# Optimization experiments

Hardware: AMD Instinct MI355X
Metric: run time of the kernel (lower is better)

## Reference

```python
import jax, jax.numpy as jnp
import numpy as np

N_HEADS = 16


def setup_inputs() -> dict:
    key = jax.random.key(0)
    ks = jax.random.split(key, 11)
    B, S, D = 4, 2048, 1024
    scale = 1.0 / np.sqrt(D)
    inp = {
        "xq": jax.random.normal(ks[0], (B, S, D), jnp.float32),
        "xk": jax.random.normal(ks[1], (B, S, D), jnp.float32),
        "xv": jax.random.normal(ks[2], (B, S, D), jnp.float32),
        "wq": jax.random.normal(ks[3], (D, D), jnp.float32) * scale,
        "bq": jnp.zeros((D,), jnp.float32),
        "wk": jax.random.normal(ks[4], (D, D), jnp.float32) * scale,
        "bk": jnp.zeros((D,), jnp.float32),
        "wv": jax.random.normal(ks[5], (D, D), jnp.float32) * scale,
        "bv": jnp.zeros((D,), jnp.float32),
        "wo": jax.random.normal(ks[6], (D, D), jnp.float32) * scale,
        "bo": jnp.zeros((D,), jnp.float32),
    }
    return inp


def reference(xq, xk, xv, wq, bq, wk, bk, wv, bv, wo, bo):
    B, S, D = xq.shape
    H = N_HEADS
    dh = D // H

    def split_heads(x):
        # (B, S, D) -> (B, H, S, dh)
        return x.reshape(B, S, H, dh).transpose(0, 2, 1, 3)

    q = split_heads(xq @ wq + bq)
    k = split_heads(xk @ wk + bk)
    v = split_heads(xv @ wv + bv)

    # FFT-based autocorrelation along the sequence axis (axis=2)
    q_fft = jnp.fft.rfft(q, axis=2)
    k_fft = jnp.fft.rfft(k, axis=2)
    autocorr = jnp.fft.irfft(q_fft * jnp.conj(k_fft), n=S, axis=2)  # (B,H,S,dh)
    scaled = autocorr / jnp.sqrt(jnp.float32(dh))

    # top-k delay selection over mean correlation across channel dim
    k_top = max(S // 5, 1)
    mean_corr = scaled.mean(axis=-1)  # (B,H,S)
    top_values, top_indices = jax.lax.top_k(mean_corr, k_top)  # (B,H,K)

    # gather values at top delays: (B,H,K,dh)
    v_sel = jnp.take_along_axis(v, top_indices[..., None], axis=2)
    weights = jax.nn.softmax(top_values, axis=-1)  # (B,H,K)
    attended = jnp.einsum('bhk,bhkd->bhd', weights, v_sel)  # (B,H,dh)

    # broadcast across seq, merge heads, output projection
    out = jnp.broadcast_to(attended[:, :, None, :], (B, H, S, dh))
    out = out.transpose(0, 2, 1, 3).reshape(B, S, D)
    return out @ wo + bo
```

## Files before the change

### kernel.cpp

```cpp
#include <hip/hip_runtime.h>
#include <math.h>

#define SB 4
#define SS 2048
#define SD 1024
#define SH 16
#define KTOP 409
#define KSL 8
#define KPS 52

typedef float f32x4  __attribute__((ext_vector_type(4)));
typedef short bf16x8 __attribute__((ext_vector_type(8)));
typedef short s16x4  __attribute__((ext_vector_type(4)));

__device__ __forceinline__ short f2bf(float x) {
  unsigned u = __float_as_uint(x);
  u += 0x7fff + ((u >> 16) & 1);
  return (short)(u >> 16);
}
__device__ __forceinline__ float bf2f(short s) {
  return __uint_as_float(((unsigned)(unsigned short)s) << 16);
}

__device__ __forceinline__ void gld16(const void* g, void* l) {
  __builtin_amdgcn_global_load_lds(
      (const __attribute__((address_space(1))) void*)g,
      (__attribute__((address_space(3))) void*)l, 16, 0, 0);
}

#define XS(i) ((i) ^ ((((i) >> 4) ^ ((i) >> 8)) & 15))

template<int SIGN>
__device__ __forceinline__ void fft2048_lds(float2* z, const float2* tw, int tid) {
#pragma unroll
  for (int l = 0; l < 4; ++l) {
    int bf = tid + l * 256;
    int i0 = XS(2 * bf), i1 = XS(2 * bf + 1);
    float2 a = z[i0], b = z[i1];
    z[i0] = make_float2(a.x + b.x, a.y + b.y);
    z[i1] = make_float2(a.x - b.x, a.y - b.y);
  }
  __syncthreads();
#pragma unroll
  for (int lq = 1; lq <= 9; lq += 2) {
    const int q = 1 << lq;
#pragma unroll
    for (int l = 0; l < 2; ++l) {
      int bf = tid + l * 256;
      int p = bf & (q - 1);
      int base = ((bf >> lq) << (lq + 2)) + p;
      int e1 = p << (9 - lq);
      int e2 = e1 << 1;
      int e3 = e1 * 3;
      float2 w1 = tw[XS(e1)];
      float2 w2 = tw[XS(e2)];
      float s3 = 1.f; int e3w = e3;
      if (e3 >= 1024) { e3w = e3 - 1024; s3 = -1.f; }
      float2 w3 = tw[XS(e3w)]; w3.x *= s3; w3.y *= s3;
      float2 t0 = z[XS(base)];
      float2 vb = z[XS(base + 2 * q)];
      float2 vc = z[XS(base + q)];
      float2 vd = z[XS(base + 3 * q)];
      float w1i = SIGN * w1.y, w2i = SIGN * w2.y, w3i = SIGN * w3.y;
      float2 t1 = make_float2(vb.x * w1.x - vb.y * w1i, vb.x * w1i + vb.y * w1.x);
      float2 t2 = make_float2(vc.x * w2.x - vc.y * w2i, vc.x * w2i + vc.y * w2.x);
      float2 t3 = make_float2(vd.x * w3.x - vd.y * w3i, vd.x * w3i + vd.y * w3.x);
      float2 s02 = make_float2(t0.x + t2.x, t0.y + t2.y);
      float2 d02 = make_float2(t0.x - t2.x, t0.y - t2.y);
      float2 s13 = make_float2(t1.x + t3.x, t1.y + t3.y);
      float2 d13 = make_float2(t1.x - t3.x, t1.y - t3.y);
      float2 r13 = make_float2(SIGN * d13.y, -SIGN * d13.x);
      z[XS(base)]         = make_float2(s02.x + s13.x, s02.y + s13.y);
      z[XS(base + q)]     = make_float2(d02.x + r13.x, d02.y + r13.y);
      z[XS(base + 2 * q)] = make_float2(s02.x - s13.x, s02.y - s13.y);
      z[XS(base + 3 * q)] = make_float2(d02.x - r13.x, d02.y - r13.y);
    }
    __syncthreads();
  }
}

template<int SIGN>
__device__ __forceinline__ void fft2048x2_lds(
    float2* __restrict__ z0, float2* __restrict__ z1,
    const float2* tw, int tid)
{
#pragma unroll
  for (int l = 0; l < 4; ++l) {
    int bf = tid + l * 256;
    int i0 = XS(2 * bf), i1 = XS(2 * bf + 1);
    float2 a0 = z0[i0], b0 = z0[i1];
    float2 a1 = z1[i0], b1 = z1[i1];
    z0[i0] = make_float2(a0.x + b0.x, a0.y + b0.y);
    z0[i1] = make_float2(a0.x - b0.x, a0.y - b0.y);
    z1[i0] = make_float2(a1.x + b1.x, a1.y + b1.y);
    z1[i1] = make_float2(a1.x - b1.x, a1.y - b1.y);
  }
  __syncthreads();
#pragma unroll
  for (int lq = 1; lq <= 9; lq += 2) {
    const int q = 1 << lq;
#pragma unroll
    for (int l = 0; l < 2; ++l) {
      int bf = tid + l * 256;
      int p = bf & (q - 1);
      int base = ((bf >> lq) << (lq + 2)) + p;
      int e1 = p << (9 - lq);
      int e2 = e1 << 1;
      int e3 = e1 * 3;
      float2 w1 = tw[XS(e1)];
      float2 w2 = tw[XS(e2)];
      float s3 = 1.f; int e3w = e3;
      if (e3 >= 1024) { e3w = e3 - 1024; s3 = -1.f; }
      float2 w3 = tw[XS(e3w)]; w3.x *= s3; w3.y *= s3;
      float w1i = SIGN * w1.y, w2i = SIGN * w2.y, w3i = SIGN * w3.y;
      const int ia = XS(base), ib = XS(base + 2 * q),
                ic = XS(base + q), id = XS(base + 3 * q);
#pragma unroll
      for (int s = 0; s < 2; ++s) {
        float2* z = s ? z1 : z0;
        float2 t0 = z[ia];
        float2 vb = z[ib];
        float2 vc = z[ic];
        float2 vd = z[id];
        float2 t1 = make_float2(vb.x * w1.x - vb.y * w1i, vb.x * w1i + vb.y * w1.x);
        float2 t2 = make_float2(vc.x * w2.x - vc.y * w2i, vc.x * w2i + vc.y * w2.x);
        float2 t3 = make_float2(vd.x * w3.x - vd.y * w3i, vd.x * w3i + vd.y * w3.x);
        float2 s02 = make_float2(t0.x + t2.x, t0.y + t2.y);
        float2 d02 = make_float2(t0.x - t2.x, t0.y - t2.y);
        float2 s13 = make_float2(t1.x + t3.x, t1.y + t3.y);
        float2 d13 = make_float2(t1.x - t3.x, t1.y - t3.y);
        float2 r13 = make_float2(SIGN * d13.y, -SIGN * d13.x);
        z[ia] = make_float2(s02.x + s13.x, s02.y + s13.y);
        z[ic] = make_float2(d02.x + r13.x, d02.y + r13.y);
        z[ib] = make_float2(s02.x - s13.x, s02.y - s13.y);
        z[id] = make_float2(d02.x - r13.x, d02.y - r13.y);
      }
    }
    __syncthreads();
  }
}

__global__ __launch_bounds__(256) void twiddle_k(float2* __restrict__ twtab) {
  int j = blockIdx.x * 256 + threadIdx.x;
  float a = 6.2831853071795864769f * (float)j / 2048.0f;
  twtab[j] = make_float2(cosf(a), -sinf(a));
}

__global__ __launch_bounds__(256) void splitwt_k(
    const float* __restrict__ wq, const float* __restrict__ wk,
    short* __restrict__ wqt, short* __restrict__ wkt)
{
  const float* W = blockIdx.z ? wk : wq;
  short* Wt = blockIdx.z ? wkt : wqt;
  const int n0 = blockIdx.x * 64, k0 = blockIdx.y * 64;
  __shared__ float T[64][65];
  const int tid = threadIdx.x;
#pragma unroll
  for (int l = 0; l < 4; ++l) {
    int idx = tid + l * 256;
    int r = idx >> 4, c4 = (idx & 15) << 2;
    float4 v = *(const float4*)&W[(size_t)(k0 + r) * SD + n0 + c4];
    T[r][c4 + 0] = v.x; T[r][c4 + 1] = v.y; T[r][c4 + 2] = v.z; T[r][c4 + 3] = v.w;
  }
  __syncthreads();
#pragma unroll
  for (int l = 0; l < 4; ++l) {
    int idx = tid + l * 256;
    int nr = idx >> 4, k4 = (idx & 15) << 2;
    s16x4 hi, lo;
#pragma unroll
    for (int j = 0; j < 4; ++j) {
      float x = T[k4 + j][nr];
      short hb = f2bf(x);
      hi[j] = hb; lo[j] = f2bf(x - bf2f(hb));
    }
    int ks = (((k4 >> 3) ^ (nr & 7)) << 3) | (k4 & 7);
    *(s16x4*)&Wt[(size_t)(n0 + nr) * 2048 + k0 + ks] = hi;
    *(s16x4*)&Wt[(size_t)(n0 + nr) * 2048 + 1024 + k0 + ks] = lo;
  }
}

__global__ __launch_bounds__(256) void splitx2_k(
    const float* __restrict__ Xq, const float* __restrict__ Xk,
    short* __restrict__ Xqh, short* __restrict__ Xql,
    short* __restrict__ Xkh, short* __restrict__ Xkl)
{
  const int tid = threadIdx.x;
  const int row = blockIdx.x * 2 + (tid >> 7);
  const int G = tid & 127;
  const float* X = blockIdx.y ? Xk : Xq;
  short* Xh = blockIdx.y ? Xkh : Xqh;
  short* Xl = blockIdx.y ? Xkl : Xql;
  const float* src = X + ((size_t)row << 10) + (G << 3);
  float4 a = *(const float4*)src;
  float4 b = *(const float4*)(src + 4);
  float xs[8] = {a.x, a.y, a.z, a.w, b.x, b.y, b.z, b.w};
  bf16x8 hi, lo;
#pragma unroll
  for (int j = 0; j < 8; ++j) {
    short hb = f2bf(xs[j]);
    hi[j] = hb; lo[j] = f2bf(xs[j] - bf2f(hb));
  }
  int Gd = (G & 0x78) | ((G ^ row) & 7);
  size_t d = ((size_t)row << 10) + (Gd << 3);
  *(bf16x8*)&Xh[d] = hi;
  *(bf16x8*)&Xl[d] = lo;
}

__global__ __launch_bounds__(256) void projm_k(
    const short* __restrict__ Xqh, const short* __restrict__ Xql,
    const short* __restrict__ Wq_, const float* __restrict__ bq_,
    float* __restrict__ Oq_,
    const short* __restrict__ Xkh, const short* __restrict__ Xkl,
    const short* __restrict__ Wk_, const float* __restrict__ bk_,
    float* __restrict__ Ok_, int ldT)
{
  const int total = gridDim.x * gridDim.y * gridDim.z;
  int g = blockIdx.x + gridDim.x * (blockIdx.y + gridDim.y * blockIdx.z);
  int t = ((total & 7) == 0) ? (((g & 7) * (total >> 3)) + (g >> 3)) : g;
  const int nb = t % gridDim.x;
  int tmp = t / gridDim.x;
  const int mb = tmp % gridDim.y;
  const int zb = tmp / gridDim.y;

  const short* Xh; const short* Xl; const short* Wt; const float* bias; float* Out;
  if (zb == 0) { Xh = Xqh; Xl = Xql; Wt = Wq_; bias = bq_; Out = Oq_; }
  else         { Xh = Xkh; Xl = Xkl; Wt = Wk_; bias = bk_; Out = Ok_; }
  const int n0 = nb * 128, m0 = mb * 128;
  __shared__ __align__(16) short Ah[128 * 64];
  __shared__ __align__(16) short Al[128 * 64];
  __shared__ __align__(16) short Bh[128 * 64];
  __shared__ __align__(16) short Bl[128 * 64];
  const int tid = threadIdx.x;
  const int wave = tid >> 6, lane = tid & 63, l15 = lane & 15, kq = lane >> 4;
  const int wr = wave >> 1, wc = wave & 1;
  const int sr = lane >> 3, sc = lane & 7;
  f32x4 acc[4][4];
#pragma unroll
  for (int i = 0; i < 4; ++i)
#pragma unroll
    for (int j = 0; j < 4; ++j)
#pragma unroll
      for (int r = 0; r < 4; ++r) acc[i][j][r] = 0.f;
  float bval[4];
#pragma unroll
  for (int j = 0; j < 4; ++j) bval[j] = bias[n0 + wc * 64 + j * 16 + l15];

  for (int s = 0; s < 16; ++s) {
    __syncthreads();
#pragma unroll
    for (int l = 0; l < 4; ++l) {
      int rr = l * 32 + wave * 8 + sr;
      int lofs = (l * 32 + wave * 8) * 64;
      size_t gA = ((size_t)(m0 + rr) << 10) + (s << 6) + (sc << 3);
      gld16(Xh + gA, Ah + lofs);
      gld16(Xl + gA, Al + lofs);
      size_t gB = ((size_t)(n0 + rr) << 11) + (s << 6) + (sc << 3);
      gld16(Wt + gB, Bh + lofs);
      gld16(Wt + gB + 1024, Bl + lofs);
    }
    __syncthreads();
#pragma unroll
    for (int ks = 0; ks < 2; ++ks) {
      int seg = ks * 4 + kq;
      bf16x8 ah[4], al[4], bh[4], bl[4];
#pragma unroll
      for (int i = 0; i < 4; ++i) {
        int ar = wr * 64 + i * 16 + l15;
        int addr = ar * 64 + ((seg ^ (ar & 7)) << 3);
        ah[i] = *(const bf16x8*)&Ah[addr];
        al[i] = *(const bf16x8*)&Al[addr];
      }
#pragma unroll
      for (int j = 0; j < 4; ++j) {
        int br = wc * 64 + j * 16 + l15;
        int addr = br * 64 + ((seg ^ (br & 7)) << 3);
        bh[j] = *(const bf16x8*)&Bh[addr];
        bl[j] = *(const bf16x8*)&Bl[addr];
      }
#pragma unroll
      for (int i = 0; i < 4; ++i)
#pragma unroll
        for (int j = 0; j < 4; ++j) {
          acc[i][j] = __builtin_amdgcn_mfma_f32_16x16x32_bf16(ah[i], bh[j], acc[i][j], 0, 0, 0);
          acc[i][j] = __builtin_amdgcn_mfma_f32_16x16x32_bf16(al[i], bh[j], acc[i][j], 0, 0, 0);
          acc[i][j] = __builtin_amdgcn_mfma_f32_16x16x32_bf16(ah[i], bl[j], acc[i][j], 0, 0, 0);
        }
    }
  }
#pragma unroll
  for (int i = 0; i < 4; ++i)
#pragma unroll
    for (int j = 0; j < 4; ++j) {
      int n = n0 + wc * 64 + j * 16 + l15;
      int tb = m0 + wr * 64 + i * 16 + kq * 4;
      float4 v = make_float4(acc[i][j][0] + bval[j], acc[i][j][1] + bval[j],
                             acc[i][j][2] + bval[j], acc[i][j][3] + bval[j]);
      *(float4*)&Out[(size_t)n * ldT + tb] = v;
    }
}

__global__ __launch_bounds__(256) void fftcorr_k(
    const float* __restrict__ Qt, const float* __restrict__ Kt,
    float* __restrict__ Pat, float2* __restrict__ Ppart,
    const float2* __restrict__ twtab, int ld)
{
  const int dg = blockIdx.x, h = blockIdx.y, b = blockIdx.z;
  const size_t bofs = (size_t)b * SS;
  __shared__ float2 z0[2048];
  __shared__ float2 z1[2048];
  __shared__ float2 tw[1024];
  const int tid = threadIdx.x;
  for (int j = tid; j < 1024; j += 256) tw[XS(j)] = twtab[j];
  float prr[8], pii[8];
#pragma unroll
  for (int l = 0; l < 8; ++l) { prr[l] = 0.f; pii[l] = 0.f; }

  for (int dd = 0; dd < 4; ++dd) {
    const int n = h * 64 + dg * 8 + dd * 2;
    const float2* q0 = (const float2*)(Qt + (size_t)n * ld + bofs);
    const float2* k0 = (const float2*)(Kt + (size_t)n * ld + bofs);
    const float2* q1 = (const float2*)(Qt + (size_t)(n + 1) * ld + bofs);
    const float2* k1 = (const float2*)(Kt + (size_t)(n + 1) * ld + bofs);
    __syncthreads();
#pragma unroll
    for (int l = 0; l < 4; ++l) {
      int t2 = tid + l * 256;
      int t = 2 * t2;
      int rv = __brev((unsigned)t) >> 21;
      int zia = XS(rv);
      int zib = XS(rv + 1024);
      float2 fq0 = q0[t2], fk0 = k0[t2];
      float2 fq1 = q1[t2], fk1 = k1[t2];
      z0[zia] = make_float2(fq0.x, fk0.x);
      z0[zib] = make_float2(fq0.y, fk0.y);
      z1[zia] = make_float2(fq1.x, fk1.x);
      z1[zib] = make_float2(fq1.y, fk1.y);
    }
    __syncthreads();
    fft2048x2_lds<1>(z0, z1, tw, tid);
#pragma unroll
    for (int l = 0; l < 8; ++l) {
      int f = tid + l * 256;
      int fc = (2048 - f) & 2047;
#pragma unroll
      for (int s = 0; s < 2; ++s) {
        const float2* z = s ? z1 : z0;
        float2 Z = z[XS(f)];
        float2 Zc = z[XS(fc)];
        float Zcr = Zc.x, Zci = -Zc.y;
        float Qr = 0.5f * (Z.x + Zcr), Qi = 0.5f * (Z.y + Zci);
        float Kr = 0.5f * (Z.y - Zci), Ki = -0.5f * (Z.x - Zcr);
        prr[l] += Qr * Kr + Qi * Ki;
        pii[l] += Qi * Kr - Qr * Ki;
      }
    }
  }
  if (Ppart) {
    float2* Pp = Ppart + ((size_t)dg * 64 + (size_t)b * SH + h) * 2048;
#pragma unroll
    for (int l = 0; l < 8; ++l) {
      int f = tid + l * 256;
      Pp[f] = make_float2(prr[l], pii[l]);
    }
  } else {
    float* Pb = Pat;
#pragma unroll
    for (int l = 0; l < 8; ++l) {
      int f = tid + l * 256;
      atomicAdd(&Pb[((size_t)h * SS + f) * 2 + 0], prr[l]);
      atomicAdd(&Pb[((size_t)h * SS + f) * 2 + 1], pii[l]);
    }
  }
}

__global__ __launch_bounds__(256) void ifft_topk_k(
    const float* __restrict__ P, const float2* __restrict__ Ppart, int nparts,
    const float2* __restrict__ twtab,
    int* __restrict__ sidx, float* __restrict__ sw)
{
  const int bh = blockIdx.x;
  __shared__ float2 z[2048];
  __shared__ float2 tw[1024];
  __shared__ unsigned keys[2048];
  __shared__ int el_i[KTOP];
  __shared__ float el_w[KTOP];
  __shared__ int hist[256];
  __shared__ int scan_sh[256];
  __shared__ int wtot[4];
  __shared__ int cnt2, tiecnt, sel_v;
  __shared__ unsigned kmax_sh;
  __shared__ float Zsh;
  const int tid = threadIdx.x;
  const int lane = tid & 63, wv = tid >> 6;
  const float SCL = 1.0f / (2048.0f * 512.0f);

  for (int j = tid; j < 1024; j += 256) tw[XS(j)] = twtab[j];
  if (tid == 0) { cnt2 = 0; tiecnt = 0; kmax_sh = 0u; Zsh = 0.f; }
#pragma unroll
  for (int l = 0; l < 8; ++l) {
    int f = tid + l * 256;
    int rv = __brev((unsigned)f) >> 21;
    float2 acc;
    if (nparts > 0) {
      acc = make_float2(0.f, 0.f);
      for (int g = 0; g < nparts; ++g) {
        float2 v = Ppart[((size_t)g * 64 + bh) * 2048 + f];
        acc.x += v.x; acc.y += v.y;
      }
    } else {
      acc = ((const float2*)P)[(size_t)bh * SS + f];
    }
    z[XS(rv)] = acc;
  }
  __syncthreads();
  fft2048_lds<-1>(z, tw, tid);

  unsigned lm = 0u;
#pragma unroll
  for (int l = 0; l < 8; ++l) {
    int i = tid + l * 256;
    float v = z[XS(i)].x * SCL;
    z[XS(i)].x = v;
    unsigned u = __float_as_uint(v);
    unsigned k = (u & 0x80000000u) ? ~u : (u | 0x80000000u);
    keys[i] = k;
    lm = max(lm, k);
  }
  atomicMax(&kmax_sh, lm);
  __syncthreads();

  unsigned prefix = 0u;
  int remaining = KTOP;
  for (int p = 3; p >= 0; --p) {
    hist[tid] = 0;
    __syncthreads();
    unsigned mask_hi = (p == 3) ? 0u : (0xFFFFFFFFu << ((p + 1) * 8));
#pragma unroll
    for (int l = 0; l < 8; ++l) {
      unsigned k = keys[tid + l * 256];
      if ((k & mask_hi) == prefix) atomicAdd(&hist[(k >> (p * 8)) & 255], 1);
    }
    __syncthreads();
    int v = hist[tid];
#pragma unroll
    for (int off2 = 1; off2 < 64; off2 <<= 1) {
      int t = __shfl_down(v, off2);
      if (lane + off2 < 64) v += t;
    }
    if (lane == 0) wtot[wv] = v;
    __syncthreads();
    for (int w = wv + 1; w < 4; ++w) v += wtot[w];
    scan_sh[tid] = v;
    __syncthreads();
    if (scan_sh[tid] >= remaining && (tid == 255 || scan_sh[tid + 1] < remaining))
      sel_v = tid;
    __syncthreads();
    int vsel = sel_v;
    int above = (vsel == 255) ? 0 : scan_sh[vsel + 1];
    remaining -= above;
    prefix |= ((unsigned)vsel) << (p * 8);
    __syncthreads();
  }
  const unsigned T = prefix;
  unsigned km = kmax_sh;
  float vmax = __uint_as_float((km & 0x80000000u) ? (km ^ 0x80000000u) : ~km);

#pragma unroll
  for (int l = 0; l < 8; ++l) {
    int i = tid + l * 256;
    unsigned k = keys[i];
    if (k > T) {
      int pos = atomicAdd(&cnt2, 1);
      el_i[pos] = i;
      el_w[pos] = expf(z[XS(i)].x - vmax);
    } else if (k == T) {
      atomicAdd(&tiecnt, 1);
    }
  }
  __syncthreads();
  int need = KTOP - cnt2;
  if (tiecnt == need) {
#pragma unroll
    for (int l = 0; l < 8; ++l) {
      int i = tid + l * 256;
      if (keys[i] == T) {
        int pos = atomicAdd(&cnt2, 1);
        el_i[pos] = i;
        el_w[pos] = expf(z[XS(i)].x - vmax);
      }
    }
  } else if (tid == 0) {
    int pos = cnt2;
    for (int i = 0; i < SS && pos < KTOP; ++i)
      if (keys[i] == T) { el_i[pos] = i; el_w[pos] = expf(z[XS(i)].x - vmax); ++pos; }
  }
  __syncthreads();
  float zs = 0.f;
  for (int l = tid; l < KTOP; l += 256) zs += el_w[l];
  atomicAdd(&Zsh, zs);
  __syncthreads();
  float invZ = 1.0f / Zsh;
  for (int l = tid; l < KTOP; l += 256) {
    sidx[bh * KTOP + l] = el_i[l];
    sw[bh * KTOP + l]   = el_w[l] * invZ;
  }
}

__global__ __launch_bounds__(256) void xbar_k(
    const int* __restrict__ sidx, const float* __restrict__ sw,
    const float* __restrict__ xv, float* __restrict__ xbar)
{
  const int bh = blockIdx.x, b = bh >> 4, sl = blockIdx.y;
  const int r0 = sl * KPS;
  const int nr = min(KTOP - r0, KPS);
  __shared__ int il[KPS];
  __shared__ float wl[KPS];
  const int tid = threadIdx.x;
  if (tid < KPS) {
    il[tid] = (tid < nr) ? sidx[bh * KTOP + r0 + tid] : 0;
    wl[tid] = (tid < nr) ? sw[bh * KTOP + r0 + tid] : 0.f;
  }
  __syncthreads();
  const float4* xv4 = (const float4*)xv;
  float4 acc = make_float4(0.f, 0.f, 0.f, 0.f);
#pragma unroll 4
  for (int r = 0; r < KPS; ++r) {
    float w = wl[r];
    float4 v = xv4[(size_t)(b * SS + il[r]) * 256 + tid];
    acc.x += w * v.x; acc.y += w * v.y; acc.z += w * v.z; acc.w += w * v.w;
  }
  float* dst = xbar + (size_t)bh * 1024 + tid * 4;
  atomicAdd(dst + 0, acc.x); atomicAdd(dst + 1, acc.y);
  atomicAdd(dst + 2, acc.z); atomicAdd(dst + 3, acc.w);
}

__global__ __launch_bounds__(256) void initbias_k(
    const float* __restrict__ bv, const float* __restrict__ bo,
    float* __restrict__ att, float* __restrict__ orow)
{
  int i = blockIdx.x * 256 + threadIdx.x;
  if (i < 4096) att[i] = bv[i & 1023];
  else          orow[i - 4096] = bo[i & 1023];
}

__global__ __launch_bounds__(256) void attend_k(
    const float* __restrict__ xbar, const float* __restrict__ wv,
    float* __restrict__ att)
{
  const int b = blockIdx.y, i0 = blockIdx.x * 64;
  __shared__ float xs[16 * 64];
  const int tid = threadIdx.x;
#pragma unroll
  for (int l = 0; l < 4; ++l) {
    int f = tid + l * 256;
    xs[f] = xbar[(size_t)(b * 16 + (f >> 6)) * 1024 + i0 + (f & 63)];
  }
  __syncthreads();
  const float4* wv4 = (const float4*)wv;
  const int h = tid >> 4;
  float4 acc = make_float4(0.f, 0.f, 0.f, 0.f);
  for (int m = 0; m < 64; ++m) {
    float xvs = xs[h * 64 + m];
    float4 w = wv4[(size_t)(i0 + m) * 256 + tid];
    acc.x += xvs * w.x; acc.y += xvs * w.y; acc.z += xvs * w.z; acc.w += xvs * w.w;
  }
  float* dst = att + (size_t)b * 1024 + tid * 4;
  atomicAdd(dst + 0, acc.x); atomicAdd(dst + 1, acc.y);
  atomicAdd(dst + 2, acc.z); atomicAdd(dst + 3, acc.w);
}

__global__ __launch_bounds__(256) void oproj_k(
    const float* __restrict__ att, const float* __restrict__ wo,
    float* __restrict__ orow)
{
  const int b = blockIdx.y, m0 = blockIdx.x * 64;
  __shared__ float as_[64];
  const int tid = threadIdx.x;
  if (tid < 64) as_[tid] = att[(size_t)b * 1024 + m0 + tid];
  __syncthreads();
  const float4* wo4 = (const float4*)wo;
  float4 acc = make_float4(0.f, 0.f, 0.f, 0.f);
  for (int m = 0; m < 64; ++m) {
    float a = as_[m];
    float4 w = wo4[(size_t)(m0 + m) * 256 + tid];
    acc.x += a * w.x; acc.y += a * w.y; acc.z += a * w.z; acc.w += a * w.w;
  }
  float* dst = orow + (size_t)b * 1024 + tid * 4;
  atomicAdd(dst + 0, acc.x); atomicAdd(dst + 1, acc.y);
  atomicAdd(dst + 2, acc.z); atomicAdd(dst + 3, acc.w);
}

__global__ __launch_bounds__(256) void bcast_k(
    const float* __restrict__ orow, float* __restrict__ out)
{
  int idx = blockIdx.x * 256 + threadIdx.x;
  const float4* o4 = (const float4*)orow;
  ((float4*)out)[idx] = o4[((idx >> 19) << 8) | (idx & 255)];
}

extern "C" void kernel_launch(void* const* d_in, const int* in_sizes, int n_in,
                              void* d_out, int out_size, void* d_ws, size_t ws_size,
                              hipStream_t stream) {
  (void)in_sizes; (void)n_in; (void)out_size;
  const float* xq = (const float*)d_in[0];
  const float* xk = (const float*)d_in[1];
  const float* xv = (const float*)d_in[2];
  const float* wq = (const float*)d_in[3];
  const float* bq = (const float*)d_in[4];
  const float* wk = (const float*)d_in[5];
  const float* bk = (const float*)d_in[6];
  const float* wv = (const float*)d_in[7];
  const float* bv = (const float*)d_in[8];
  const float* wo = (const float*)d_in[9];
  const float* bo = (const float*)d_in[10];
  float* out = (float*)d_out;

  char* base = (char*)d_ws;
  float* P = (float*)base;
  size_t off = (size_t)SB * SH * SS * 2 * 4;
  float2* twtab = (float2*)(base + off); off += 1024 * 8;
  int*   sidx = (int*)  (base + off); off += (size_t)SB * SH * KTOP * 4;
  float* sw   = (float*)(base + off); off += (size_t)SB * SH * KTOP * 4;
  float* xbar = (float*)(base + off); off += (size_t)SB * SH * SD * 4;
  float* att  = (float*)(base + off); off += (size_t)SB * SD * 4;
  float* orow = (float*)(base + off); off += (size_t)SB * SD * 4;

  size_t big0 = (off + 1048575) & ~(size_t)1048575;
  const size_t SZ_X = (size_t)SB * SS * SD * 2;
  const size_t SZ_T = (size_t)SD * SB * SS * 4;
  const size_t SZ_W = (size_t)SD * 2048 * 2;
  const size_t SZ_P = (size_t)8 * 64 * 2048 * 8;
  size_t need_big = big0 + 4 * SZ_X + 2 * SZ_T + 2 * SZ_W + SZ_P;

  twiddle_k<<<dim3(4), 256, 0, stream>>>(twtab);
  hipMemsetAsync(xbar, 0, (size_t)SB * SH * SD * sizeof(float), stream);

  if (ws_size >= need_big) {
    char* bb = base + big0;
    short* Xqh = (short*)(bb);
    short* Xql = (short*)(bb + SZ_X);
    short* Xkh = (short*)(bb + 2 * SZ_X);
    short* Xkl = (short*)(bb + 3 * SZ_X);
    float* Qt  = (float*)(bb + 4 * SZ_X);
    float* Kt  = (float*)(bb + 4 * SZ_X + SZ_T);
    short* Wqt = (short*)(bb + 4 * SZ_X + 2 * SZ_T);
    short* Wkt = (short*)(bb + 4 * SZ_X + 2 * SZ_T + SZ_W);
    float2* Pp = (float2*)(bb + 4 * SZ_X + 2 * SZ_T + 2 * SZ_W);

    splitwt_k<<<dim3(16, 16, 2), 256, 0, stream>>>(wq, wk, Wqt, Wkt);
    splitx2_k<<<dim3(SB * SS / 2, 2), 256, 0, stream>>>(xq, xk, Xqh, Xql, Xkh, Xkl);
    projm_k<<<dim3(8, SB * SS / 128, 2), 256, 0, stream>>>(
        Xqh, Xql, Wqt, bq, Qt, Xkh, Xkl, Wkt, bk, Kt, SB * SS);
    fftcorr_k<<<dim3(8, 16, SB), 256, 0, stream>>>(
        Qt, Kt, nullptr, Pp, twtab, SB * SS);
    ifft_topk_k<<<dim3(SB * SH), 256, 0, stream>>>(P, Pp, 8, twtab, sidx, sw);
  } else {
    char* ob = (char*)d_out;
    float* Qt  = (float*)(ob);
    float* Kt  = (float*)(ob + ( 8u << 20));
    short* Wqt = (short*)(ob + (16u << 20));
    short* Wkt = (short*)(ob + (20u << 20));
    short* Xh  = (short*)(ob + (24u << 20));
    short* Xl  = (short*)(ob + (28u << 20));

    hipMemsetAsync(P, 0, (size_t)SB * SH * SS * 2 * sizeof(float), stream);
    splitwt_k<<<dim3(16, 16, 2), 256, 0, stream>>>(wq, wk, Wqt, Wkt);
    for (int b = 0; b < SB; ++b) {
      const float* xqb = xq + (size_t)b * SS * SD;
      const float* xkb = xk + (size_t)b * SS * SD;
      splitx2_k<<<dim3(SS / 2, 1), 256, 0, stream>>>(xqb, xqb, Xh, Xl, Xh, Xl);
      projm_k<<<dim3(8, SS / 128, 1), 256, 0, stream>>>(
          Xh, Xl, Wqt, bq, Qt, Xh, Xl, Wqt, bq, Qt, SS);
      splitx2_k<<<dim3(SS / 2, 1), 256, 0, stream>>>(xkb, xkb, Xh, Xl, Xh, Xl);
      projm_k<<<dim3(8, SS / 128, 1), 256, 0, stream>>>(
          Xh, Xl, Wkt, bk, Kt, Xh, Xl, Wkt, bk, Kt, SS);
      fftcorr_k<<<dim3(8, 16, 1), 256, 0, stream>>>(
          Qt, Kt, P + (size_t)b * SH * SS * 2, nullptr, twtab, SS);
    }
    ifft_topk_k<<<dim3(SB * SH), 256, 0, stream>>>(P, nullptr, 0, twtab, sidx, sw);
  }

  xbar_k<<<dim3(SB * SH, KSL), 256, 0, stream>>>(sidx, sw, xv, xbar);
  initbias_k<<<dim3(32), 256, 0, stream>>>(bv, bo, att, orow);
  attend_k<<<dim3(16, SB), 256, 0, stream>>>(xbar, wv, att);
  oproj_k<<<dim3(16, SB), 256, 0, stream>>>(att, wo, orow);
  bcast_k<<<dim3(8192), 256, 0, stream>>>(orow, out);
}
```

Measured before the change: 369.6 us.

## Inline twiddle generation, prefetch FFT inputs, replace xbar atomics with partials

Removes the separate twiddle kernel by computing twiddles in LDS inside fftcorr_k and ifft_topk_k. It also drops the memset in the fast path, so two launches disappear. In fftcorr_k, the next channel pair's global loads are issued into registers before the current FFT runs, overlapping memory latency with compute. xbar_k now writes per-slice partials to a workspace buffer that attend_k sums, replacing float atomics and the memset. The cost is extra sin/cos work per block, more registers, and a larger workspace requirement.

```diff
diff --git a/kernel.cpp b/kernel.cpp
--- a/kernel.cpp
+++ b/kernel.cpp
@@ -140,10 +140,11 @@
   }
 }
 
-__global__ __launch_bounds__(256) void twiddle_k(float2* __restrict__ twtab) {
-  int j = blockIdx.x * 256 + threadIdx.x;
-  float a = 6.2831853071795864769f * (float)j / 2048.0f;
-  twtab[j] = make_float2(cosf(a), -sinf(a));
+__device__ __forceinline__ void build_tw(float2* tw, int tid) {
+  for (int j = tid; j < 1024; j += 256) {
+    float a = 6.2831853071795864769f * (float)j / 2048.0f;
+    tw[XS(j)] = make_float2(cosf(a), -sinf(a));
+  }
 }
 
 __global__ __launch_bounds__(256) void splitwt_k(
@@ -302,8 +303,7 @@
 
 __global__ __launch_bounds__(256) void fftcorr_k(
     const float* __restrict__ Qt, const float* __restrict__ Kt,
-    float* __restrict__ Pat, float2* __restrict__ Ppart,
-    const float2* __restrict__ twtab, int ld)
+    float* __restrict__ Pat, float2* __restrict__ Ppart, int ld)
 {
   const int dg = blockIdx.x, h = blockIdx.y, b = blockIdx.z;
   const size_t bofs = (size_t)b * SS;
@@ -311,17 +311,26 @@
   __shared__ float2 z1[2048];
   __shared__ float2 tw[1024];
   const int tid = threadIdx.x;
-  for (int j = tid; j < 1024; j += 256) tw[XS(j)] = twtab[j];
+  build_tw(tw, tid);
   float prr[8], pii[8];
 #pragma unroll
   for (int l = 0; l < 8; ++l) { prr[l] = 0.f; pii[l] = 0.f; }
 
-  for (int dd = 0; dd < 4; ++dd) {
-    const int n = h * 64 + dg * 8 + dd * 2;
+  float2 rq0[4], rk0[4], rq1[4], rk1[4];
+  {
+    const int n = h * 64 + dg * 8;
     const float2* q0 = (const float2*)(Qt + (size_t)n * ld + bofs);
     const float2* k0 = (const float2*)(Kt + (size_t)n * ld + bofs);
     const float2* q1 = (const float2*)(Qt + (size_t)(n + 1) * ld + bofs);
     const float2* k1 = (const float2*)(Kt + (size_t)(n + 1) * ld + bofs);
+#pragma unroll
+    for (int l = 0; l < 4; ++l) {
+      int t2 = tid + l * 256;
+      rq0[l] = q0[t2]; rk0[l] = k0[t2]; rq1[l] = q1[t2]; rk1[l] = k1[t2];
+    }
+  }
+
+  for (int dd = 0; dd < 4; ++dd) {
     __syncthreads();
 #pragma unroll
     for (int l = 0; l < 4; ++l) {
@@ -330,12 +339,22 @@
       int rv = __brev((unsigned)t) >> 21;
       int zia = XS(rv);
       int zib = XS(rv + 1024);
-      float2 fq0 = q0[t2], fk0 = k0[t2];
-      float2 fq1 = q1[t2], fk1 = k1[t2];
-      z0[zia] = make_float2(fq0.x, fk0.x);
-      z0[zib] = make_float2(fq0.y, fk0.y);
-      z1[zia] = make_float2(fq1.x, fk1.x);
-      z1[zib] = make_float2(fq1.y, fk1.y);
+      z0[zia] = make_float2(rq0[l].x, rk0[l].x);
+      z0[zib] = make_float2(rq0[l].y, rk0[l].y);
+      z1[zia] = make_float2(rq1[l].x, rk1[l].x);
+      z1[zib] = make_float2(rq1[l].y, rk1[l].y);
+    }
+    if (dd < 3) {
+      const int n = h * 64 + dg * 8 + (dd + 1) * 2;
+      const float2* q0 = (const float2*)(Qt + (size_t)n * ld + bofs);
+      const float2* k0 = (const float2*)(Kt + (size_t)n * ld + bofs);
+      const float2* q1 = (const float2*)(Qt + (size_t)(n + 1) * ld + bofs);
+      const float2* k1 = (const float2*)(Kt + (size_t)(n + 1) * ld + bofs);
+#pragma unroll
+      for (int l = 0; l < 4; ++l) {
+        int t2 = tid + l * 256;
+        rq0[l] = q0[t2]; rk0[l] = k0[t2]; rq1[l] = q1[t2]; rk1[l] = k1[t2];
+      }
     }
     __syncthreads();
     fft2048x2_lds<1>(z0, z1, tw, tid);
@@ -376,7 +395,6 @@
 
 __global__ __launch_bounds__(256) void ifft_topk_k(
     const float* __restrict__ P, const float2* __restrict__ Ppart, int nparts,
-    const float2* __restrict__ twtab,
     int* __restrict__ sidx, float* __restrict__ sw)
 {
   const int bh = blockIdx.x;
@@ -395,7 +413,7 @@
   const int lane = tid & 63, wv = tid >> 6;
   const float SCL = 1.0f / (2048.0f * 512.0f);
 
-  for (int j = tid; j < 1024; j += 256) tw[XS(j)] = twtab[j];
+  build_tw(tw, tid);
   if (tid == 0) { cnt2 = 0; tiecnt = 0; kmax_sh = 0u; Zsh = 0.f; }
 #pragma unroll
   for (int l = 0; l < 8; ++l) {
@@ -509,7 +527,8 @@
 
 __global__ __launch_bounds__(256) void xbar_k(
     const int* __restrict__ sidx, const float* __restrict__ sw,
-    const float* __restrict__ xv, float* __restrict__ xbar)
+    const float* __restrict__ xv, float* __restrict__ xbar,
+    float* __restrict__ xpart)
 {
   const int bh = blockIdx.x, b = bh >> 4, sl = blockIdx.y;
   const int r0 = sl * KPS;
@@ -530,9 +549,13 @@
     float4 v = xv4[(size_t)(b * SS + il[r]) * 256 + tid];
     acc.x += w * v.x; acc.y += w * v.y; acc.z += w * v.z; acc.w += w * v.w;
   }
-  float* dst = xbar + (size_t)bh * 1024 + tid * 4;
-  atomicAdd(dst + 0, acc.x); atomicAdd(dst + 1, acc.y);
-  atomicAdd(dst + 2, acc.z); atomicAdd(dst + 3, acc.w);
+  if (xpart) {
+    ((float4*)(xpart + ((size_t)sl * 64 + bh) * 1024))[tid] = acc;
+  } else {
+    float* dst = xbar + (size_t)bh * 1024 + tid * 4;
+    atomicAdd(dst + 0, acc.x); atomicAdd(dst + 1, acc.y);
+    atomicAdd(dst + 2, acc.z); atomicAdd(dst + 3, acc.w);
+  }
 }
 
 __global__ __launch_bounds__(256) void initbias_k(
@@ -545,8 +568,8 @@
 }
 
 __global__ __launch_bounds__(256) void attend_k(
-    const float* __restrict__ xbar, const float* __restrict__ wv,
-    float* __restrict__ att)
+    const float* __restrict__ xbar, const float* __restrict__ xpart, int nsl,
+    const float* __restrict__ wv, float* __restrict__ att)
 {
   const int b = blockIdx.y, i0 = blockIdx.x * 64;
   __shared__ float xs[16 * 64];
@@ -554,7 +577,16 @@
 #pragma unroll
   for (int l = 0; l < 4; ++l) {
     int f = tid + l * 256;
-    xs[f] = xbar[(size_t)(b * 16 + (f >> 6)) * 1024 + i0 + (f & 63)];
+    int hh = f >> 6, ii = i0 + (f & 63);
+    float s;
+    if (nsl > 0) {
+      s = 0.f;
+      for (int g = 0; g < nsl; ++g)
+        s += xpart[((size_t)g * 64 + b * 16 + hh) * 1024 + ii];
+    } else {
+      s = xbar[(size_t)(b * 16 + hh) * 1024 + ii];
+    }
+    xs[f] = s;
   }
   __syncthreads();
   const float4* wv4 = (const float4*)wv;
@@ -619,7 +651,6 @@
   char* base = (char*)d_ws;
   float* P = (float*)base;
   size_t off = (size_t)SB * SH * SS * 2 * 4;
-  float2* twtab = (float2*)(base + off); off += 1024 * 8;
   int*   sidx = (int*)  (base + off); off += (size_t)SB * SH * KTOP * 4;
   float* sw   = (float*)(base + off); off += (size_t)SB * SH * KTOP * 4;
   float* xbar = (float*)(base + off); off += (size_t)SB * SH * SD * 4;
@@ -631,10 +662,8 @@
   const size_t SZ_T = (size_t)SD * SB * SS * 4;
   const size_t SZ_W = (size_t)SD * 2048 * 2;
   const size_t SZ_P = (size_t)8 * 64 * 2048 * 8;
-  size_t need_big = big0 + 4 * SZ_X + 2 * SZ_T + 2 * SZ_W + SZ_P;
-
-  twiddle_k<<<dim3(4), 256, 0, stream>>>(twtab);
-  hipMemsetAsync(xbar, 0, (size_t)SB * SH * SD * sizeof(float), stream);
+  const size_t SZ_XP = (size_t)KSL * 64 * 1024 * 4;
+  size_t need_big = big0 + 4 * SZ_X + 2 * SZ_T + 2 * SZ_W + SZ_P + SZ_XP;
 
   if (ws_size >= need_big) {
     char* bb = base + big0;
@@ -647,14 +676,17 @@
     short* Wqt = (short*)(bb + 4 * SZ_X + 2 * SZ_T);
     short* Wkt = (short*)(bb + 4 * SZ_X + 2 * SZ_T + SZ_W);
     float2* Pp = (float2*)(bb + 4 * SZ_X + 2 * SZ_T + 2 * SZ_W);
+    float* Xpart = (float*)(bb + 4 * SZ_X + 2 * SZ_T + 2 * SZ_W + SZ_P);
 
     splitwt_k<<<dim3(16, 16, 2), 256, 0, stream>>>(wq, wk, Wqt, Wkt);
     splitx2_k<<<dim3(SB * SS / 2, 2), 256, 0, stream>>>(xq, xk, Xqh, Xql, Xkh, Xkl);
     projm_k<<<dim3(8, SB * SS / 128, 2), 256, 0, stream>>>(
         Xqh, Xql, Wqt, bq, Qt, Xkh, Xkl, Wkt, bk, Kt, SB * SS);
-    fftcorr_k<<<dim3(8, 16, SB), 256, 0, stream>>>(
-        Qt, Kt, nullptr, Pp, twtab, SB * SS);
-    ifft_topk_k<<<dim3(SB * SH), 256, 0, stream>>>(P, Pp, 8, twtab, sidx, sw);
+    fftcorr_k<<<dim3(8, 16, SB), 256, 0, stream>>>(Qt, Kt, nullptr, Pp, SB * SS);
+    ifft_topk_k<<<dim3(SB * SH), 256, 0, stream>>>(P, Pp, 8, sidx, sw);
+    xbar_k<<<dim3(SB * SH, KSL), 256, 0, stream>>>(sidx, sw, xv, nullptr, Xpart);
+    initbias_k<<<dim3(32), 256, 0, stream>>>(bv, bo, att, orow);
+    attend_k<<<dim3(16, SB), 256, 0, stream>>>(nullptr, Xpart, KSL, wv, att);
   } else {
     char* ob = (char*)d_out;
     float* Qt  = (float*)(ob);
@@ -665,6 +697,7 @@
     short* Xl  = (short*)(ob + (28u << 20));
 
     hipMemsetAsync(P, 0, (size_t)SB * SH * SS * 2 * sizeof(float), stream);
+    hipMemsetAsync(xbar, 0, (size_t)SB * SH * SD * sizeof(float), stream);
     splitwt_k<<<dim3(16, 16, 2), 256, 0, stream>>>(wq, wk, Wqt, Wkt);
     for (int b = 0; b < SB; ++b) {
       const float* xqb = xq + (size_t)b * SS * SD;
@@ -676,14 +709,14 @@
       projm_k<<<dim3(8, SS / 128, 1), 256, 0, stream>>>(
           Xh, Xl, Wkt, bk, Kt, Xh, Xl, Wkt, bk, Kt, SS);
       fftcorr_k<<<dim3(8, 16, 1), 256, 0, stream>>>(
-          Qt, Kt, P + (size_t)b * SH * SS * 2, nullptr, twtab, SS);
-    }
-    ifft_topk_k<<<dim3(SB * SH), 256, 0, stream>>>(P, nullptr, 0, twtab, sidx, sw);
-  }
-
-  xbar_k<<<dim3(SB * SH, KSL), 256, 0, stream>>>(sidx, sw, xv, xbar);
-  initbias_k<<<dim3(32), 256, 0, stream>>>(bv, bo, att, orow);
-  attend_k<<<dim3(16, SB), 256, 0, stream>>>(xbar, wv, att);
+          Qt, Kt, P + (size_t)b * SH * SS * 2, nullptr, SS);
+    }
+    ifft_topk_k<<<dim3(SB * SH), 256, 0, stream>>>(P, nullptr, 0, sidx, sw);
+    xbar_k<<<dim3(SB * SH, KSL), 256, 0, stream>>>(sidx, sw, xv, xbar, nullptr);
+    initbias_k<<<dim3(32), 256, 0, stream>>>(bv, bo, att, orow);
+    attend_k<<<dim3(16, SB), 256, 0, stream>>>(xbar, nullptr, 0, wv, att);
+  }
+
   oproj_k<<<dim3(16, SB), 256, 0, stream>>>(att, wo, orow);
   bcast_k<<<dim3(8192), 256, 0, stream>>>(orow, out);
 }
```

Measured after the change: 353.3 us, median of 2. 1.05x faster.
